# Kernel optimization log

Measured on AMD Instinct MI355X. Metric: run time of the kernel, lower is better.

## Reference

```python
import jax, jax.numpy as jnp
import numpy as np
from jax import lax

B, NMEAS, M, LAYER_NUM = 2048, 128, 256, 10
CLAMP_MIN, CLAMP_MAX = 1e-6, 100.0
EPS_S = 1e-6


def _conv2d(x, w, b):
    y = lax.conv_general_dilated(x, w, (1, 1), 'SAME', dimension_numbers=('NCHW', 'OIHW', 'NCHW'))
    return y + b[None, :, None, None]


def _conv1d(x, w, b):
    y = lax.conv_general_dilated(x, w, (1,), 'SAME', dimension_numbers=('NCH', 'OIH', 'NCH'))
    return y + b[None, :, None]


def setup_inputs():
    key = jax.random.key(0)
    ks = jax.random.split(key, 12)
    s = 1.0 / np.sqrt(2.0 * NMEAS)  # ~unit-norm dictionary columns
    return {
        'Yr': jax.random.normal(ks[0], (B, 1, NMEAS, 1), jnp.float32),
        'Yi': jax.random.normal(ks[1], (B, 1, NMEAS, 1), jnp.float32),
        'Ar': s * jax.random.normal(ks[2], (NMEAS, M), jnp.float32),
        'Ai': s * jax.random.normal(ks[3], (NMEAS, M), jnp.float32),
        'conv1_w': 0.1 * jax.random.normal(ks[4], (32, 2, 3, 3), jnp.float32),
        'conv1_b': jnp.zeros((32,), jnp.float32),
        'conv2_w': 0.1 * jax.random.normal(ks[5], (64, 32, 3, 3), jnp.float32),
        'conv2_b': jnp.zeros((64,), jnp.float32),
        'hc_w': 0.1 * jax.random.normal(ks[6], (LAYER_NUM - 1, 64, 3), jnp.float32),
        'hc_b': jnp.zeros((LAYER_NUM - 1,), jnp.float32),
        'hd_w': 0.1 * jax.random.normal(ks[7], (LAYER_NUM - 1, 64, 3), jnp.float32),
        'hd_b': jnp.zeros((LAYER_NUM - 1,), jnp.float32),
        'hT_w': 0.1 * jax.random.normal(ks[8], (LAYER_NUM, 64, 3), jnp.float32),
        'hT_b': jnp.zeros((LAYER_NUM,), jnp.float32),
        'a0': jnp.asarray(1.0, jnp.float32),
        'b0': jnp.asarray(1.0, jnp.float32),
    }


def _hypernet(ay, c1w, c1b, c2w, c2b, hcw, hcb, hdw, hdb, hTw, hTb):
    # ay: [B, 2, M]; batch acts as image width (context)
    x_img = jnp.transpose(ay, (1, 2, 0))[None]              # [1, 2, M, B]
    f = jax.nn.relu(_conv2d(x_img, c1w, c1b))               # [1, 32, M, B]
    f = jax.nn.relu(_conv2d(f, c2w, c2b))                   # [1, 64, M, B]
    f = jnp.mean(f, axis=2)                                 # AdaptiveAvgPool2d((1,None)) -> [1, 64, B]
    c = jnp.abs(_conv1d(f, hcw, hcb))[0].T                  # [B, L-1]
    d = jnp.abs(_conv1d(f, hdw, hdb))[0].T                  # [B, L-1]
    T = jnp.abs(_conv1d(f, hTw, hTb))[0].T                  # [B, L]
    c = jnp.clip(c, CLAMP_MIN, CLAMP_MAX)
    d = jnp.maximum(d, CLAMP_MIN)
    T = jnp.clip(T, CLAMP_MIN, CLAMP_MAX)
    return c, d, T


def _forward(Yr, Yi, Ar, Ai, conv1_w, conv1_b, conv2_w, conv2_b,
             hc_w, hc_b, hd_w, hd_b, hT_w, hT_b, a0, b0):
    Y = (Yr + 1j * Yi).astype(jnp.complex64)                # [B,1,Nmeas,1]
    A = (Ar + 1j * Ai).astype(jnp.complex64)                # [Nmeas,M]
    AT = A.conj().T                                         # [M,Nmeas]
    AA = AT @ A                                             # [M,M] Hermitian
    AY = jnp.matmul(AT, Y)                                  # [B,1,M,1]
    b = Y.shape[0]
    n = Y.shape[2]
    ay = jnp.concatenate([AY.real.reshape(b, 1, -1), AY.imag.reshape(b, 1, -1)], axis=1)  # [B,2,M]
    c, d, T = _hypernet(ay, conv1_w, conv1_b, conv2_w, conv2_b,
                        hc_w, hc_b, hd_w, hd_b, hT_w, hT_b)
    D = jnp.real(jnp.diagonal(AA))[None, None, :, None]     # diag of Hermitian AA is real; [1,1,M,1]
    eps = (a0 / b0).astype(jnp.complex64) * jnp.ones((b, 1, 1, 1), jnp.complex64)
    Lam = ((c[:, 0] / d[:, 0])[:, None, None, None] * jnp.ones((1, 1, M, 1), jnp.float32)).astype(jnp.complex64)
    U = jnp.zeros((b, 1, M, 1), jnp.complex64)
    a = a0 + n
    for k in range(LAYER_NUM - 1):
        Tk = T[:, k][:, None, None, None]
        # fused SBL/VAMP mean update
        U = eps * (Tk * U - jnp.matmul(AA, U) + AY) / (eps * Tk + Lam + EPS_S)
        Sigma = 1.0 / (eps * D + Lam + EPS_S)
        r = Y - jnp.matmul(A, U)
        eps1 = jnp.sum(r.real ** 2 + r.imag ** 2, axis=(2, 3), keepdims=True)  # ||.||_F^2
        eps2 = jnp.sum(D * Sigma, axis=(2, 3), keepdims=True)
        eps = a / (b0 + eps1 + eps2 + EPS_S)
        Lam = (c[:, k][:, None, None, None] + 1.0) / (
            d[:, k][:, None, None, None] + jnp.abs(U) ** 2 + Sigma + EPS_S)
    Tk = T[:, LAYER_NUM - 1][:, None, None, None]
    U = eps * (Tk * U - jnp.matmul(AA, U) + AY) / (eps * Tk + Lam + EPS_S)
    Ua = jnp.abs(U)
    Ua = Ua / (jnp.max(Ua) + 1e-8)
    return Ua, c, d, T


def reference(Yr, Yi, Ar, Ai, conv1_w, conv1_b, conv2_w, conv2_b,
              hc_w, hc_b, hd_w, hd_b, hT_w, hT_b, a0, b0):
    Ua, c, d, T = _forward(Yr, Yi, Ar, Ai, conv1_w, conv1_b, conv2_w, conv2_b,
                           hc_w, hc_b, hd_w, hd_b, hT_w, hT_b, a0, b0)
    # original returns the last batch row of c/d/T (detached diagnostics)
    return Ua, c[-1:, :], d[-1:, :], T[-1:, :]
```

## Files before the change

### kernel.cpp

```cpp
#include <hip/hip_runtime.h>
#include <math.h>

#define B_N   2048
#define NM    128
#define M_N   256
#define LNUM  10
#define EPS_Sf 1e-6f

typedef _Float16 half8 __attribute__((ext_vector_type(8)));
typedef float floatx4 __attribute__((ext_vector_type(4)));

__device__ __forceinline__ float frcp(float x) { return __builtin_amdgcn_rcpf(x); }

static constexpr size_t o_AA  = 0;
static constexpr size_t o_D   = o_AA  + 131072;
static constexpr size_t o_yn  = o_D   + 256;
static constexpr size_t o_AY  = o_yn  + 2048;
static constexpr size_t o_AYt = o_AY  + 1048576;
static constexpr size_t o_w2t = o_AYt + 1048576;
static constexpr size_t o_z1  = o_w2t + 18432;
static constexpr size_t o_fp  = o_z1  + 16777216;
static constexpr size_t o_f   = o_fp  + 2097152;
static constexpr size_t o_c   = o_f   + 131072;
static constexpr size_t o_dd  = o_c   + 18432;
static constexpr size_t o_T   = o_dd  + 18432;
static constexpr size_t o_Ua  = o_T   + 20480;
static constexpr size_t o_gm  = o_Ua  + 524288;

#define Z1T_RS (2050 * 32)

__global__ void k_pre(const float* __restrict__ Ar, const float* __restrict__ Ai,
                      const float* __restrict__ Yr, const float* __restrict__ Yi,
                      const float* __restrict__ w2, float* __restrict__ ws) {
    __shared__ float sb[2048];
    int blk = blockIdx.x;
    int tid = threadIdx.x;
    if (blk < 256) {
        float* cr = sb; float* ci = sb + NM;
        int i = blk, j = tid;
        if (j < NM) { cr[j] = Ar[j * M_N + i]; ci[j] = Ai[j * M_N + i]; }
        __syncthreads();
        float sr = 0.f, si = 0.f;
        for (int n = 0; n < NM; ++n) {
            float ar = Ar[n * M_N + j], ai = Ai[n * M_N + j];
            sr += cr[n] * ar + ci[n] * ai;
            si += cr[n] * ai - ci[n] * ar;
        }
        _Float16* A16 = (_Float16*)(ws + o_AA);
        size_t off = ((size_t)((i >> 4) * 8 + (j >> 5)) * 64
                      + (size_t)(((j >> 3) & 3) * 16 + (i & 15))) * 8 + (j & 7);
        A16[off]         = (_Float16)sr;
        A16[65536 + off] = (_Float16)si;
        if (j == i) ws[o_D + i] = sr;
        if (i == 0 && j == 0) *(unsigned int*)(ws + o_gm) = 0u;
    } else if (blk < 328) {
        int i = (blk - 256) * 256 + tid;
        if (i < 64 * 32 * 9) {
            int oc = i / 288, r = i % 288;
            int ic = r / 9, kk = r % 9;
            _Float16* Wa = (_Float16*)(ws + o_w2t);
            Wa[((size_t)oc * 9 + kk) * 32 + ic] = (_Float16)w2[i];
        }
    } else {
        float2* Ys = (float2*)sb;
        int bb0 = (blk - 328) * 8;
        for (int i = tid; i < 8 * NM; i += 256) {
            int g = i >> 7, n = i & 127;
            Ys[g * NM + n] = make_float2(Yr[(size_t)(bb0 + g) * NM + n],
                                         Yi[(size_t)(bb0 + g) * NM + n]);
        }
        __syncthreads();
        if (tid < 8) {
            float s = 0.f;
            for (int n = 0; n < NM; ++n) { float2 y = Ys[tid * NM + n]; s += y.x * y.x + y.y * y.y; }
            ws[o_yn + bb0 + tid] = s;
        }
        int m = tid;
        float accr[8], acci[8];
#pragma unroll
        for (int g = 0; g < 8; ++g) { accr[g] = 0.f; acci[g] = 0.f; }
        for (int n = 0; n < NM; ++n) {
            float ar = Ar[n * M_N + m], ai = Ai[n * M_N + m];
#pragma unroll
            for (int g = 0; g < 8; ++g) {
                float2 y = Ys[g * NM + n];
                accr[g] += ar * y.x + ai * y.y;
                acci[g] += ar * y.y - ai * y.x;
            }
        }
        float2* AY = (float2*)(ws + o_AY);
#pragma unroll
        for (int g = 0; g < 8; ++g) {
            AY[(size_t)(bb0 + g) * M_N + m] = make_float2(accr[g], acci[g]);
            ws[o_AYt + (size_t)m * B_N + (bb0 + g)] = accr[g];
            ws[o_AYt + 524288 + (size_t)m * B_N + (bb0 + g)] = acci[g];
        }
    }
}

__global__ void k_conv1(const float* __restrict__ w1, const float* __restrict__ b1,
                        float* __restrict__ ws) {
    __shared__ float w1s[576], b1s[32];
    int tid = threadIdx.x;
    for (int i = tid; i < 576; i += 256) w1s[i] = w1[i];
    if (tid < 32) b1s[tid] = b1[tid];
    __syncthreads();
    int gidx = blockIdx.x * 256 + tid;
    int b = gidx & (B_N - 1), m = gidx >> 11;
    const float* xr = ws + o_AYt;
    float x[2][3][3];
#pragma unroll
    for (int c = 0; c < 2; ++c)
#pragma unroll
        for (int dm = 0; dm < 3; ++dm) {
            int mm = m + dm - 1;
#pragma unroll
            for (int db = 0; db < 3; ++db) {
                int bb = b + db - 1;
                x[c][dm][db] = (mm >= 0 && mm < M_N && bb >= 0 && bb < B_N)
                                 ? xr[(size_t)c * 524288 + (size_t)mm * B_N + bb] : 0.f;
            }
        }
    _Float16* z1t = (_Float16*)(ws + o_z1);
    _Float16 zv[32];
    for (int oc = 0; oc < 32; ++oc) {
        float acc = b1s[oc];
#pragma unroll
        for (int c = 0; c < 2; ++c)
#pragma unroll
            for (int dm = 0; dm < 3; ++dm)
#pragma unroll
                for (int db = 0; db < 3; ++db)
                    acc += x[c][dm][db] * w1s[oc * 18 + c * 9 + dm * 3 + db];
        zv[oc] = (_Float16)fmaxf(acc, 0.f);
    }
    _Float16* dst = z1t + (size_t)(m + 1) * Z1T_RS + (size_t)(b + 1) * 32;
#pragma unroll
    for (int v = 0; v < 4; ++v) *(half8*)(dst + v * 8) = *(half8*)(zv + v * 8);
    half8 z8 = (half8)((_Float16)0.f);
    if (m == 0) {
        _Float16* d2 = z1t + (size_t)(b + 1) * 32;
#pragma unroll
        for (int v = 0; v < 4; ++v) *(half8*)(d2 + v * 8) = z8;
        if (b == 0) { _Float16* d3 = z1t;
#pragma unroll
            for (int v = 0; v < 4; ++v) *(half8*)(d3 + v * 8) = z8; }
        if (b == B_N - 1) { _Float16* d3 = z1t + (size_t)2049 * 32;
#pragma unroll
            for (int v = 0; v < 4; ++v) *(half8*)(d3 + v * 8) = z8; }
    }
    if (m == M_N - 1) {
        _Float16* d2 = z1t + (size_t)257 * Z1T_RS + (size_t)(b + 1) * 32;
#pragma unroll
        for (int v = 0; v < 4; ++v) *(half8*)(d2 + v * 8) = z8;
        if (b == 0) { _Float16* d3 = z1t + (size_t)257 * Z1T_RS;
#pragma unroll
            for (int v = 0; v < 4; ++v) *(half8*)(d3 + v * 8) = z8; }
        if (b == B_N - 1) { _Float16* d3 = z1t + (size_t)257 * Z1T_RS + (size_t)2049 * 32;
#pragma unroll
            for (int v = 0; v < 4; ++v) *(half8*)(d3 + v * 8) = z8; }
    }
    if (b == 0) {
        _Float16* d2 = z1t + (size_t)(m + 1) * Z1T_RS;
#pragma unroll
        for (int v = 0; v < 4; ++v) *(half8*)(d2 + v * 8) = z8;
    }
    if (b == B_N - 1) {
        _Float16* d2 = z1t + (size_t)(m + 1) * Z1T_RS + (size_t)2049 * 32;
#pragma unroll
        for (int v = 0; v < 4; ++v) *(half8*)(d2 + v * 8) = z8;
    }
}

#define MFMA16(A,Bv,C) C = __builtin_amdgcn_mfma_f32_16x16x32_f16(A, Bv, C, 0, 0, 0)
__global__ void __launch_bounds__(128)
k_conv2m(const float* __restrict__ b2, float* __restrict__ ws) {
    int tid = threadIdx.x;
    int lane = tid & 63, wv = tid >> 6;
    int col = lane & 15, quad = lane >> 4;
    int bt = blockIdx.x & 127, g = blockIdx.x >> 7;
    int b0 = bt * 16, m0 = g * 16;
    int oc0w = wv * 32;
    const _Float16* z1t = (const _Float16*)(ws + o_z1);
    const _Float16* Wa  = (const _Float16*)(ws + o_w2t);

    half8 Af[2][9];
#pragma unroll
    for (int t = 0; t < 2; ++t)
#pragma unroll
        for (int kk = 0; kk < 9; ++kk)
            Af[t][kk] = *(const half8*)(Wa + ((size_t)(oc0w + t * 16 + col) * 9 + kk) * 32 + quad * 8);
    float bias[2][4];
#pragma unroll
    for (int t = 0; t < 2; ++t)
#pragma unroll
        for (int r = 0; r < 4; ++r)
            bias[t][r] = b2[oc0w + t * 16 + quad * 4 + r];

    const _Float16* zb = z1t + (size_t)(b0 + col) * 32 + quad * 8;
    half8 Bf[3][3];
#pragma unroll
    for (int ph = 0; ph < 3; ++ph)
#pragma unroll
        for (int db = 0; db < 3; ++db)
            Bf[ph][db] = *(const half8*)(zb + (size_t)(m0 + ph) * Z1T_RS + (size_t)db * 32);

    floatx4 facc[2];
    facc[0] = (floatx4){0.f, 0.f, 0.f, 0.f};
    facc[1] = (floatx4){0.f, 0.f, 0.f, 0.f};

#pragma unroll
    for (int mm = 0; mm < 16; ++mm) {
        floatx4 a0 = (floatx4){0.f, 0.f, 0.f, 0.f};
        floatx4 a1 = (floatx4){0.f, 0.f, 0.f, 0.f};
#pragma unroll
        for (int dm = 0; dm < 3; ++dm) {
            int ph = (mm + dm) % 3;
#pragma unroll
            for (int db = 0; db < 3; ++db) {
                MFMA16(Af[0][dm * 3 + db], Bf[ph][db], a0);
                MFMA16(Af[1][dm * 3 + db], Bf[ph][db], a1);
            }
        }
#pragma unroll
        for (int r = 0; r < 4; ++r) {
            facc[0][r] += fmaxf(a0[r] + bias[0][r], 0.f);
            facc[1][r] += fmaxf(a1[r] + bias[1][r], 0.f);
        }
        if (mm < 15) {
            int ph = mm % 3;
#pragma unroll
            for (int db = 0; db < 3; ++db)
                Bf[ph][db] = *(const half8*)(zb + (size_t)(m0 + mm + 3) * Z1T_RS + (size_t)db * 32);
        }
    }
    float* fp = ws + o_fp + (size_t)g * 131072;
#pragma unroll
    for (int t = 0; t < 2; ++t)
#pragma unroll
        for (int r = 0; r < 4; ++r)
            fp[(size_t)(oc0w + t * 16 + quad * 4 + r) * B_N + b0 + col] = facc[t][r];
}

__global__ void k_fred(float* __restrict__ ws) {
    size_t i = (size_t)blockIdx.x * 256 + threadIdx.x;
    float s = 0.f;
    for (int p = 0; p < 16; ++p) s += ws[o_fp + (size_t)p * 131072 + i];
    ws[o_f + i] = s * (1.f / 256.f);
}

__global__ void k_cdt(const float* __restrict__ hcw, const float* __restrict__ hcb,
                      const float* __restrict__ hdw, const float* __restrict__ hdb,
                      const float* __restrict__ hTw, const float* __restrict__ hTb,
                      float* __restrict__ ws, float* __restrict__ out) {
    int l = blockIdx.x >> 3;
    int b = (blockIdx.x & 7) * 256 + threadIdx.x;
    const float* f = ws + o_f;
    const float* w; float bi; int li, kind;
    if (l < 9)       { kind = 0; li = l;      w = hcw + (size_t)li * 192; bi = hcb[li]; }
    else if (l < 18) { kind = 1; li = l - 9;  w = hdw + (size_t)li * 192; bi = hdb[li]; }
    else             { kind = 2; li = l - 18; w = hTw + (size_t)li * 192; bi = hTb[li]; }
    __shared__ float wsm[192];
    for (int i = threadIdx.x; i < 192; i += 256) wsm[i] = w[i];
    __syncthreads();
    float acc = bi;
    bool okL = (b > 0), okR = (b < B_N - 1);
    for (int ic = 0; ic < 64; ++ic) {
        const float* fr = f + (size_t)ic * B_N + b;
        float fm1 = okL ? fr[-1] : 0.f;
        float f0  = fr[0];
        float fp1 = okR ? fr[1] : 0.f;
        acc += fm1 * wsm[ic * 3] + f0 * wsm[ic * 3 + 1] + fp1 * wsm[ic * 3 + 2];
    }
    float v = fmaxf(fabsf(acc), 1e-6f);
    if (kind != 1) v = fminf(v, 100.f);
    if (kind == 0)      { ws[o_c  + (size_t)b * 9  + li] = v; if (b == B_N - 1) out[524288 + li] = v; }
    else if (kind == 1) { ws[o_dd + (size_t)b * 9  + li] = v; if (b == B_N - 1) out[524297 + li] = v; }
    else                { ws[o_T  + (size_t)b * 10 + li] = v; if (b == B_N - 1) out[524306 + li] = v; }
}

__global__ void __launch_bounds__(1024, 4)
k_iter(const float* __restrict__ a0p, const float* __restrict__ b0p, float* __restrict__ ws) {
    __shared__ __align__(16) _Float16 Ubf[2][8][64][8];
    __shared__ __align__(16) float redv[16][52];
    __shared__ float redm[16];
    int tid = threadIdx.x;
    int lane = tid & 63, w = tid >> 6;
    int col = lane & 15, quad = lane >> 4;
    int b = blockIdx.x * 16 + col;
    const float2* AY = (const float2*)(ws + o_AY);
    const _Float16* Af = (const _Float16*)(ws + o_AA);
    float a0 = a0p[0], b0v = b0p[0];
    float atot = a0 + (float)NM;
    float yn = ws[o_yn + b];
    float eps = a0 / b0v;
    float Tv[10], cv[9], dvv[9];
#pragma unroll
    for (int i = 0; i < 10; ++i) Tv[i] = ws[o_T + (size_t)b * 10 + i];
#pragma unroll
    for (int i = 0; i < 9; ++i) cv[i] = ws[o_c + (size_t)b * 9 + i];
#pragma unroll
    for (int i = 0; i < 9; ++i) dvv[i] = ws[o_dd + (size_t)b * 9 + i];
    float lam0 = cv[0] * frcp(dvv[0]);
    half8 Ar8[8], Ai8[8];
#pragma unroll
    for (int ks = 0; ks < 8; ++ks) {
        const _Float16* ab = Af + ((size_t)(w * 8 + ks) * 64 + lane) * 8;
        Ar8[ks] = *(const half8*)(ab);
        Ai8[ks] = *(const half8*)(ab + 65536);
    }
    float Dv[4], ayr[4], ayi[4], lam[4], Ur[4], Ui[4], sg[4], wr_[4], wi_[4];
#pragma unroll
    for (int r = 0; r < 4; ++r) {
        int m = w * 16 + quad * 4 + r;
        Dv[r] = ws[o_D + m];
        float2 a = AY[(size_t)b * M_N + m];
        ayr[r] = a.x; ayi[r] = a.y;
        lam[r] = lam0;
        Ur[r] = 0.f; Ui[r] = 0.f; wr_[r] = 0.f; wi_[r] = 0.f;
    }
    int ksw = w >> 1;
    int quadD = (w & 1) * 2 + (quad >> 1);
    int laneD = quadD * 16 + col;
    int eb = (quad & 1) * 4;
    for (int k = 0; k < LNUM; ++k) {
        float Tk = Tv[k];
#pragma unroll
        for (int r = 0; r < 4; ++r) {
            float iv = eps * frcp(fmaf(eps, Tk, lam[r] + EPS_Sf));
            Ur[r] = iv * (Tk * Ur[r] - wr_[r] + ayr[r]);
            Ui[r] = iv * (Tk * Ui[r] - wi_[r] + ayi[r]);
        }
        if (k == LNUM - 1) break;
        {
            union { _Float16 h[4]; unsigned long long u; } c0, c2;
#pragma unroll
            for (int r = 0; r < 4; ++r) {
                c0.h[r] = (_Float16)Ur[r];
                c2.h[r] = (_Float16)Ui[r];
            }
            *(unsigned long long*)&Ubf[0][ksw][laneD][eb] = c0.u;
            *(unsigned long long*)&Ubf[1][ksw][laneD][eb] = c2.u;
        }
        __syncthreads();
        floatx4 wrp = (floatx4){0.f, 0.f, 0.f, 0.f};
        floatx4 wrn = (floatx4){0.f, 0.f, 0.f, 0.f};
        floatx4 wia1 = (floatx4){0.f, 0.f, 0.f, 0.f};
        floatx4 wia2 = (floatx4){0.f, 0.f, 0.f, 0.f};
#pragma unroll
        for (int ks = 0; ks < 8; ++ks) {
            half8 urh = *(const half8*)&Ubf[0][ks][lane][0];
            half8 uih = *(const half8*)&Ubf[1][ks][lane][0];
            MFMA16(Ar8[ks], urh, wrp);
            MFMA16(Ai8[ks], uih, wrn);
            MFMA16(Ar8[ks], uih, wia1);
            MFMA16(Ai8[ks], urh, wia2);
        }
        float p1 = 0.f, p2 = 0.f, p3 = 0.f;
#pragma unroll
        for (int r = 0; r < 4; ++r) {
            wr_[r] = wrp[r] - wrn[r];
            wi_[r] = wia1[r] + wia2[r];
            sg[r] = frcp(fmaf(eps, Dv[r], lam[r] + EPS_Sf));
            p1 += ayr[r] * Ur[r] + ayi[r] * Ui[r];
            p2 += Ur[r] * wr_[r] + Ui[r] * wi_[r];
            p3 += Dv[r] * sg[r];
        }
        p1 += __shfl_xor(p1, 16); p1 += __shfl_xor(p1, 32);
        p2 += __shfl_xor(p2, 16); p2 += __shfl_xor(p2, 32);
        p3 += __shfl_xor(p3, 16); p3 += __shfl_xor(p3, 32);
        if (lane < 16) {
            redv[col][w * 3]     = p1;
            redv[col][w * 3 + 1] = p2;
            redv[col][w * 3 + 2] = p3;
        }
        __syncthreads();
        float s[3] = {0.f, 0.f, 0.f};
#pragma unroll
        for (int j = 0; j < 12; ++j) {
            floatx4 v4 = *(const floatx4*)&redv[col][j * 4];
#pragma unroll
            for (int e = 0; e < 4; ++e) s[(j * 4 + e) % 3] += v4[e];
        }
        float eps1 = fmaxf(yn - 2.f * s[0] + s[1], 0.f);
        eps = atot * frcp(b0v + eps1 + s[2] + EPS_Sf);
        float ck1 = cv[k] + 1.f;
        float dk = dvv[k];
#pragma unroll
        for (int r = 0; r < 4; ++r)
            lam[r] = ck1 * frcp(dk + Ur[r] * Ur[r] + Ui[r] * Ui[r] + sg[r] + EPS_Sf);
    }
    float4 v;
    v.x = sqrtf(Ur[0] * Ur[0] + Ui[0] * Ui[0]);
    v.y = sqrtf(Ur[1] * Ur[1] + Ui[1] * Ui[1]);
    v.z = sqrtf(Ur[2] * Ur[2] + Ui[2] * Ui[2]);
    v.w = sqrtf(Ur[3] * Ur[3] + Ui[3] * Ui[3]);
    *(float4*)&ws[o_Ua + (size_t)b * M_N + w * 16 + quad * 4] = v;
    float lm = fmaxf(fmaxf(v.x, v.y), fmaxf(v.z, v.w));
#pragma unroll
    for (int off = 32; off >= 1; off >>= 1) lm = fmaxf(lm, __shfl_xor(lm, off));
    if (lane == 0) redm[w] = lm;
    __syncthreads();
    if (tid == 0) {
        float mx = redm[0];
#pragma unroll
        for (int i = 1; i < 16; ++i) mx = fmaxf(mx, redm[i]);
        atomicMax((unsigned int*)(ws + o_gm), __float_as_uint(mx));
    }
}

__global__ void k_norm(const float* __restrict__ ws, float* __restrict__ out) {
    size_t i = (size_t)blockIdx.x * 256 + threadIdx.x;
    float gm = __uint_as_float(*(const unsigned int*)(ws + o_gm));
    out[i] = ws[o_Ua + i] / (gm + 1e-8f);
}

extern "C" void kernel_launch(void* const* d_in, const int* in_sizes, int n_in,
                              void* d_out, int out_size, void* d_ws, size_t ws_size,
                              hipStream_t stream) {
    (void)in_sizes; (void)n_in; (void)out_size; (void)ws_size;
    const float* Yr  = (const float*)d_in[0];
    const float* Yi  = (const float*)d_in[1];
    const float* Ar  = (const float*)d_in[2];
    const float* Ai  = (const float*)d_in[3];
    const float* w1  = (const float*)d_in[4];
    const float* b1  = (const float*)d_in[5];
    const float* w2  = (const float*)d_in[6];
    const float* b2  = (const float*)d_in[7];
    const float* hcw = (const float*)d_in[8];
    const float* hcb = (const float*)d_in[9];
    const float* hdw = (const float*)d_in[10];
    const float* hdb = (const float*)d_in[11];
    const float* hTw = (const float*)d_in[12];
    const float* hTb = (const float*)d_in[13];
    const float* a0  = (const float*)d_in[14];
    const float* b0  = (const float*)d_in[15];
    float* ws = (float*)d_ws;
    float* out = (float*)d_out;

    k_pre   <<<584, 256, 0, stream>>>(Ar, Ai, Yr, Yi, w2, ws);
    k_conv1 <<<2048, 256, 0, stream>>>(w1, b1, ws);
    k_conv2m<<<2048, 128, 0, stream>>>(b2, ws);
    k_fred  <<<512, 256, 0, stream>>>(ws);
    k_cdt   <<<224, 256, 0, stream>>>(hcw, hcb, hdw, hdb, hTw, hTb, ws, out);
    k_iter  <<<128, 1024, 0, stream>>>(a0, b0, ws);
    k_norm  <<<2048, 256, 0, stream>>>(ws, out);
}
```

Baseline: 225.9 us.

## Halve k_iter block to 512 threads with two M-tiles per wave

The iterative solver kernel now runs 8 waves per block instead of 16. Each wave handles two 16-row tiles of M, holding twice the A fragments in registers and issuing 8 MFMAs per k-step, which cuts block-wide barrier and reduction cost. The loop is restructured so the first U update comes from the initial zero state, and the lambda and U updates are fused at the end of each iteration. Per-iteration c, d and T values are loaded inside the loop rather than kept in registers. In exchange, register pressure per thread rises and only 128 blocks of 8 waves run, which lowers the number of waves available to hide latency.

```diff
diff --git a/kernel.cpp b/kernel.cpp
--- a/kernel.cpp
+++ b/kernel.cpp
@@ -279,93 +279,106 @@
     else                { ws[o_T  + (size_t)b * 10 + li] = v; if (b == B_N - 1) out[524306 + li] = v; }
 }
 
-__global__ void __launch_bounds__(1024, 4)
+__global__ void __launch_bounds__(512, 2)
 k_iter(const float* __restrict__ a0p, const float* __restrict__ b0p, float* __restrict__ ws) {
     __shared__ __align__(16) _Float16 Ubf[2][8][64][8];
-    __shared__ __align__(16) float redv[16][52];
-    __shared__ float redm[16];
+    __shared__ __align__(16) float redv[16][28];
+    __shared__ float redm[8];
     int tid = threadIdx.x;
     int lane = tid & 63, w = tid >> 6;
     int col = lane & 15, quad = lane >> 4;
     int b = blockIdx.x * 16 + col;
+
+    for (int i = tid; i < 16 * 28; i += 512) ((float*)redv)[i] = 0.f;
+
     const float2* AY = (const float2*)(ws + o_AY);
     const _Float16* Af = (const _Float16*)(ws + o_AA);
     float a0 = a0p[0], b0v = b0p[0];
     float atot = a0 + (float)NM;
     float yn = ws[o_yn + b];
     float eps = a0 / b0v;
-    float Tv[10], cv[9], dvv[9];
-#pragma unroll
-    for (int i = 0; i < 10; ++i) Tv[i] = ws[o_T + (size_t)b * 10 + i];
-#pragma unroll
-    for (int i = 0; i < 9; ++i) cv[i] = ws[o_c + (size_t)b * 9 + i];
-#pragma unroll
-    for (int i = 0; i < 9; ++i) dvv[i] = ws[o_dd + (size_t)b * 9 + i];
-    float lam0 = cv[0] * frcp(dvv[0]);
-    half8 Ar8[8], Ai8[8];
-#pragma unroll
-    for (int ks = 0; ks < 8; ++ks) {
-        const _Float16* ab = Af + ((size_t)(w * 8 + ks) * 64 + lane) * 8;
-        Ar8[ks] = *(const half8*)(ab);
-        Ai8[ks] = *(const half8*)(ab + 65536);
-    }
-    float Dv[4], ayr[4], ayi[4], lam[4], Ur[4], Ui[4], sg[4], wr_[4], wi_[4];
-#pragma unroll
-    for (int r = 0; r < 4; ++r) {
-        int m = w * 16 + quad * 4 + r;
-        Dv[r] = ws[o_D + m];
+
+    half8 Ar8[2][8], Ai8[2][8];
+#pragma unroll
+    for (int t = 0; t < 2; ++t)
+#pragma unroll
+        for (int ks = 0; ks < 8; ++ks) {
+            const _Float16* ab = Af + (((size_t)(w * 2 + t) * 8 + ks) * 64 + lane) * 8;
+            Ar8[t][ks] = *(const half8*)(ab);
+            Ai8[t][ks] = *(const half8*)(ab + 65536);
+        }
+
+    float Dv[8], ayr[8], ayi[8], lam[8], Ur[8], Ui[8];
+    float c0h = ws[o_c + (size_t)b * 9];
+    float d0h = ws[o_dd + (size_t)b * 9];
+    float T0 = ws[o_T + (size_t)b * 10];
+    float lam0 = c0h * frcp(d0h);
+#pragma unroll
+    for (int ri = 0; ri < 8; ++ri) {
+        int m = w * 32 + (ri >> 2) * 16 + quad * 4 + (ri & 3);
+        Dv[ri] = ws[o_D + m];
         float2 a = AY[(size_t)b * M_N + m];
-        ayr[r] = a.x; ayi[r] = a.y;
-        lam[r] = lam0;
-        Ur[r] = 0.f; Ui[r] = 0.f; wr_[r] = 0.f; wi_[r] = 0.f;
-    }
-    int ksw = w >> 1;
-    int quadD = (w & 1) * 2 + (quad >> 1);
-    int laneD = quadD * 16 + col;
+        ayr[ri] = a.x; ayi[ri] = a.y;
+        lam[ri] = lam0;
+    }
+    {
+        float iv = eps * frcp(fmaf(eps, T0, lam0 + EPS_Sf));
+#pragma unroll
+        for (int ri = 0; ri < 8; ++ri) { Ur[ri] = iv * ayr[ri]; Ui[ri] = iv * ayi[ri]; }
+    }
+
+    int laneD0 = ((quad >> 1)) * 16 + col;
+    int laneD1 = (2 + (quad >> 1)) * 16 + col;
     int eb = (quad & 1) * 4;
-    for (int k = 0; k < LNUM; ++k) {
-        float Tk = Tv[k];
-#pragma unroll
-        for (int r = 0; r < 4; ++r) {
-            float iv = eps * frcp(fmaf(eps, Tk, lam[r] + EPS_Sf));
-            Ur[r] = iv * (Tk * Ur[r] - wr_[r] + ayr[r]);
-            Ui[r] = iv * (Tk * Ui[r] - wi_[r] + ayi[r]);
-        }
-        if (k == LNUM - 1) break;
+
+    for (int k = 0; k < LNUM - 1; ++k) {
+        float ck = ws[o_c + (size_t)b * 9 + k];
+        float dk = ws[o_dd + (size_t)b * 9 + k];
+        float Tn = ws[o_T + (size_t)b * 10 + k + 1];
         {
-            union { _Float16 h[4]; unsigned long long u; } c0, c2;
-#pragma unroll
-            for (int r = 0; r < 4; ++r) {
-                c0.h[r] = (_Float16)Ur[r];
-                c2.h[r] = (_Float16)Ui[r];
+            union { _Float16 h[4]; unsigned long long u; } pk;
+#pragma unroll
+            for (int t = 0; t < 2; ++t) {
+                int ld = t ? laneD1 : laneD0;
+#pragma unroll
+                for (int r = 0; r < 4; ++r) pk.h[r] = (_Float16)Ur[t * 4 + r];
+                *(unsigned long long*)&Ubf[0][w][ld][eb] = pk.u;
+#pragma unroll
+                for (int r = 0; r < 4; ++r) pk.h[r] = (_Float16)Ui[t * 4 + r];
+                *(unsigned long long*)&Ubf[1][w][ld][eb] = pk.u;
             }
-            *(unsigned long long*)&Ubf[0][ksw][laneD][eb] = c0.u;
-            *(unsigned long long*)&Ubf[1][ksw][laneD][eb] = c2.u;
         }
         __syncthreads();
-        floatx4 wrp = (floatx4){0.f, 0.f, 0.f, 0.f};
-        floatx4 wrn = (floatx4){0.f, 0.f, 0.f, 0.f};
-        floatx4 wia1 = (floatx4){0.f, 0.f, 0.f, 0.f};
-        floatx4 wia2 = (floatx4){0.f, 0.f, 0.f, 0.f};
+        floatx4 ac[8];
+#pragma unroll
+        for (int i = 0; i < 8; ++i) ac[i] = (floatx4){0.f, 0.f, 0.f, 0.f};
 #pragma unroll
         for (int ks = 0; ks < 8; ++ks) {
             half8 urh = *(const half8*)&Ubf[0][ks][lane][0];
             half8 uih = *(const half8*)&Ubf[1][ks][lane][0];
-            MFMA16(Ar8[ks], urh, wrp);
-            MFMA16(Ai8[ks], uih, wrn);
-            MFMA16(Ar8[ks], uih, wia1);
-            MFMA16(Ai8[ks], urh, wia2);
-        }
+            MFMA16(Ar8[0][ks], urh, ac[0]);
+            MFMA16(Ai8[0][ks], uih, ac[1]);
+            MFMA16(Ar8[0][ks], uih, ac[2]);
+            MFMA16(Ai8[0][ks], urh, ac[3]);
+            MFMA16(Ar8[1][ks], urh, ac[4]);
+            MFMA16(Ai8[1][ks], uih, ac[5]);
+            MFMA16(Ar8[1][ks], uih, ac[6]);
+            MFMA16(Ai8[1][ks], urh, ac[7]);
+        }
+        float wr[8], wi[8], sg[8];
         float p1 = 0.f, p2 = 0.f, p3 = 0.f;
 #pragma unroll
-        for (int r = 0; r < 4; ++r) {
-            wr_[r] = wrp[r] - wrn[r];
-            wi_[r] = wia1[r] + wia2[r];
-            sg[r] = frcp(fmaf(eps, Dv[r], lam[r] + EPS_Sf));
-            p1 += ayr[r] * Ur[r] + ayi[r] * Ui[r];
-            p2 += Ur[r] * wr_[r] + Ui[r] * wi_[r];
-            p3 += Dv[r] * sg[r];
-        }
+        for (int t = 0; t < 2; ++t)
+#pragma unroll
+            for (int r = 0; r < 4; ++r) {
+                int ri = t * 4 + r;
+                wr[ri] = ac[t * 4 + 0][r] - ac[t * 4 + 1][r];
+                wi[ri] = ac[t * 4 + 2][r] + ac[t * 4 + 3][r];
+                sg[ri] = frcp(fmaf(eps, Dv[ri], lam[ri] + EPS_Sf));
+                p1 += ayr[ri] * Ur[ri] + ayi[ri] * Ui[ri];
+                p2 += Ur[ri] * wr[ri] + Ui[ri] * wi[ri];
+                p3 += Dv[ri] * sg[ri];
+            }
         p1 += __shfl_xor(p1, 16); p1 += __shfl_xor(p1, 32);
         p2 += __shfl_xor(p2, 16); p2 += __shfl_xor(p2, 32);
         p3 += __shfl_xor(p3, 16); p3 += __shfl_xor(p3, 32);
@@ -377,26 +390,33 @@
         __syncthreads();
         float s[3] = {0.f, 0.f, 0.f};
 #pragma unroll
-        for (int j = 0; j < 12; ++j) {
+        for (int j = 0; j < 7; ++j) {
             floatx4 v4 = *(const floatx4*)&redv[col][j * 4];
 #pragma unroll
             for (int e = 0; e < 4; ++e) s[(j * 4 + e) % 3] += v4[e];
         }
         float eps1 = fmaxf(yn - 2.f * s[0] + s[1], 0.f);
         eps = atot * frcp(b0v + eps1 + s[2] + EPS_Sf);
-        float ck1 = cv[k] + 1.f;
-        float dk = dvv[k];
-#pragma unroll
-        for (int r = 0; r < 4; ++r)
-            lam[r] = ck1 * frcp(dk + Ur[r] * Ur[r] + Ui[r] * Ui[r] + sg[r] + EPS_Sf);
-    }
-    float4 v;
-    v.x = sqrtf(Ur[0] * Ur[0] + Ui[0] * Ui[0]);
-    v.y = sqrtf(Ur[1] * Ur[1] + Ui[1] * Ui[1]);
-    v.z = sqrtf(Ur[2] * Ur[2] + Ui[2] * Ui[2]);
-    v.w = sqrtf(Ur[3] * Ur[3] + Ui[3] * Ui[3]);
-    *(float4*)&ws[o_Ua + (size_t)b * M_N + w * 16 + quad * 4] = v;
-    float lm = fmaxf(fmaxf(v.x, v.y), fmaxf(v.z, v.w));
+        float ck1 = ck + 1.f;
+#pragma unroll
+        for (int ri = 0; ri < 8; ++ri) {
+            lam[ri] = ck1 * frcp(dk + Ur[ri] * Ur[ri] + Ui[ri] * Ui[ri] + sg[ri] + EPS_Sf);
+            float iv = eps * frcp(fmaf(eps, Tn, lam[ri] + EPS_Sf));
+            Ur[ri] = iv * (Tn * Ur[ri] - wr[ri] + ayr[ri]);
+            Ui[ri] = iv * (Tn * Ui[ri] - wi[ri] + ayi[ri]);
+        }
+    }
+    float lm = 0.f;
+#pragma unroll
+    for (int t = 0; t < 2; ++t) {
+        float4 v;
+        v.x = sqrtf(Ur[t * 4 + 0] * Ur[t * 4 + 0] + Ui[t * 4 + 0] * Ui[t * 4 + 0]);
+        v.y = sqrtf(Ur[t * 4 + 1] * Ur[t * 4 + 1] + Ui[t * 4 + 1] * Ui[t * 4 + 1]);
+        v.z = sqrtf(Ur[t * 4 + 2] * Ur[t * 4 + 2] + Ui[t * 4 + 2] * Ui[t * 4 + 2]);
+        v.w = sqrtf(Ur[t * 4 + 3] * Ur[t * 4 + 3] + Ui[t * 4 + 3] * Ui[t * 4 + 3]);
+        *(float4*)&ws[o_Ua + (size_t)b * M_N + w * 32 + t * 16 + quad * 4] = v;
+        lm = fmaxf(lm, fmaxf(fmaxf(v.x, v.y), fmaxf(v.z, v.w)));
+    }
 #pragma unroll
     for (int off = 32; off >= 1; off >>= 1) lm = fmaxf(lm, __shfl_xor(lm, off));
     if (lane == 0) redm[w] = lm;
@@ -404,7 +424,7 @@
     if (tid == 0) {
         float mx = redm[0];
 #pragma unroll
-        for (int i = 1; i < 16; ++i) mx = fmaxf(mx, redm[i]);
+        for (int i = 1; i < 8; ++i) mx = fmaxf(mx, redm[i]);
         atomicMax((unsigned int*)(ws + o_gm), __float_as_uint(mx));
     }
 }
@@ -443,6 +463,6 @@
     k_conv2m<<<2048, 128, 0, stream>>>(b2, ws);
     k_fred  <<<512, 256, 0, stream>>>(ws);
     k_cdt   <<<224, 256, 0, stream>>>(hcw, hcb, hdw, hdb, hTw, hTb, ws, out);
-    k_iter  <<<128, 1024, 0, stream>>>(a0, b0, ws);
+    k_iter  <<<128, 512, 0, stream>>>(a0, b0, ws);
     k_norm  <<<2048, 256, 0, stream>>>(ws, out);
 }
```

Measured after the change: 229.4 us. Within noise of the previous version (+1.5%).
